# Performance work log

Hardware: AMD Instinct MI355X
Metric: run time of the kernel (lower is better)

The kernel has to match this reference:

```python
import jax, jax.numpy as jnp
import numpy as np

B, T, C = 4, 2048, 1024
E, D, TOP_K = 8, 3072, 2


def setup_inputs() -> dict:
    key = jax.random.key(0)
    ks = jax.random.split(key, 6)
    s_c = 1.0 / np.sqrt(C)
    s_d = 1.0 / np.sqrt(D)
    return {
        "x": jax.random.normal(ks[0], (B, T, C), dtype=jnp.float32),
        "router_w": jax.random.uniform(ks[1], (E, C), jnp.float32, -s_c, s_c),
        "W1": jax.random.uniform(ks[2], (E, C, D), jnp.float32, -s_c, s_c),
        "b1": jax.random.uniform(ks[3], (E, D), jnp.float32, -s_c, s_c),
        "W2": jax.random.uniform(ks[4], (E, D, C), jnp.float32, -s_d, s_d),
        "b2": jax.random.uniform(ks[5], (E, C), jnp.float32, -s_d, s_d),
    }


def reference(x, router_w, W1, b1, W2, b2):
    b, t, c = x.shape
    xf = x.reshape(b * t, c)                      # [N, C]
    n = xf.shape[0]
    logits = xf @ router_w.T                       # [N, E]
    probs = jax.nn.softmax(logits, axis=-1)
    topw, topi = jax.lax.top_k(probs, TOP_K)       # [N, k]
    topw = topw / jnp.sum(topw, axis=-1, keepdims=True)
    # scatter normalized top-k weights into [N, E] combine weights
    mask = jnp.zeros_like(probs).at[jnp.arange(n)[:, None], topi].set(topw)
    # dense expert MLPs (zero combine weight == token not routed to expert)
    h = jax.nn.gelu(jnp.einsum('nc,ecd->ned', xf, W1) + b1, approximate=False)
    y = jnp.einsum('ned,edc->nec', h, W2) + b2     # [N, E, C]
    out = jnp.einsum('ne,nec->nc', mask, y).reshape(b, t, c)
    aux_loss = jnp.zeros((), dtype=x.dtype)        # eval mode
    return out, aux_loss
```

## Files before the change

kernel.cpp:

```cpp
#include <hip/hip_runtime.h>
#include <math.h>

#define N_TOK 8192
#define C_DIM 1024
#define D_DIM 3072
#define E_NUM 8
#define SEG 128
#define MAXB 136

typedef unsigned short u16;
typedef unsigned int u32;
typedef __attribute__((ext_vector_type(8))) short bf16x8;
typedef __attribute__((ext_vector_type(4))) float f32x4;

__device__ __forceinline__ u16 f2bf(float f) {
  u32 u = __builtin_bit_cast(unsigned int, f);
  u = (u + 0x7FFFu + ((u >> 16) & 1u)) >> 16;
  return (u16)u;
}

__global__ void zcnt_kernel(float* __restrict__ out, int n, int* __restrict__ cnt) {
  if (threadIdx.x < E_NUM) cnt[threadIdx.x] = 0;
  const int tail = n & 3;
  if (threadIdx.x < tail) out[n - 1 - (int)threadIdx.x] = 0.0f;
}

__global__ void router_kernel(const float* __restrict__ x, const float* __restrict__ rw,
                              int* __restrict__ cnt, int* __restrict__ list,
                              float* __restrict__ wl, float* __restrict__ out) {
  const int lane = threadIdx.x & 63;
  const int n = blockIdx.x * 4 + (threadIdx.x >> 6);
  {
    float4 z = make_float4(0.f, 0.f, 0.f, 0.f);
    float* orow = out + (size_t)n * C_DIM;
#pragma unroll
    for (int i = 0; i < 4; i++) *(float4*)(orow + lane * 4 + i * 256) = z;
  }
  const float* xr = x + (size_t)n * C_DIM;
  double acc[E_NUM];
#pragma unroll
  for (int e = 0; e < E_NUM; e++) acc[e] = 0.0;
#pragma unroll
  for (int i = 0; i < 4; i++) {
    const int c = lane * 4 + i * 256;
    float4 xv = *(const float4*)(xr + c);
#pragma unroll
    for (int e = 0; e < E_NUM; e++) {
      const float* rwe = rw + e * C_DIM + c;
      acc[e] += (double)xv.x * (double)rwe[0] + (double)xv.y * (double)rwe[1]
              + (double)xv.z * (double)rwe[2] + (double)xv.w * (double)rwe[3];
    }
  }
#pragma unroll
  for (int e = 0; e < E_NUM; e++) {
    double v = acc[e];
#pragma unroll
    for (int off = 32; off > 0; off >>= 1) v += __shfl_down(v, off, 64);
    acc[e] = v;
  }
  if (lane == 0) {
    int i0 = 0;
#pragma unroll
    for (int e = 1; e < E_NUM; e++) if (acc[e] > acc[i0]) i0 = e;
    int i1 = (i0 == 0) ? 1 : 0;
#pragma unroll
    for (int e = 0; e < E_NUM; e++) if (e != i0 && acc[e] > acc[i1]) i1 = e;
    double d = acc[i0] - acc[i1];
    double w0 = 1.0 / (1.0 + exp(-d));
    double w1 = 1.0 - w0;
    int p0 = atomicAdd(&cnt[i0], 1);
    list[i0 * N_TOK + p0] = n; wl[i0 * N_TOK + p0] = (float)w0;
    int p1 = atomicAdd(&cnt[i1], 1);
    list[i1 * N_TOK + p1] = n; wl[i1 * N_TOK + p1] = (float)w1;
  }
}

template<int R, int CC>
__global__ __launch_bounds__(512) void transpose_conv_kernel(
    const float* __restrict__ in, u16* __restrict__ outp) {
  __shared__ float t[32][257];
  const int e = blockIdx.z;
  const int r0 = blockIdx.y * 32;
  const int c0 = blockIdx.x * 256;
  const int tid = threadIdx.x;
  const int lr = tid >> 6;
  const int lc = (tid & 63) * 4;
#pragma unroll
  for (int i = 0; i < 4; i++) {
    const int rr = lr + i * 8;
    float4 v = *(const float4*)(in + ((size_t)e * R + r0 + rr) * CC + c0 + lc);
    t[rr][lc] = v.x; t[rr][lc + 1] = v.y; t[rr][lc + 2] = v.z; t[rr][lc + 3] = v.w;
  }
  __syncthreads();
  const int od = tid >> 1;
  const int seg = (tid & 1) * 16;
  union { u16 s[16]; uint4 v[2]; } o;
#pragma unroll
  for (int j = 0; j < 16; j++) o.s[j] = f2bf(t[seg + j][od]);
  u16* dst = outp + ((size_t)e * CC + c0 + od) * R + r0 + seg;
  *(uint4*)(dst) = o.v[0];
  *(uint4*)(dst + 8) = o.v[1];
}

__global__ void prefix_kernel(const int* __restrict__ cnt, int* __restrict__ rowbase,
                              int* __restrict__ btab) {
  const int lane = threadIdx.x;
  int c[E_NUM], rbse[E_NUM], nseg[E_NUM], nsb[E_NUM];
  int s = 0, t = 0;
#pragma unroll
  for (int e = 0; e < E_NUM; e++) {
    c[e] = cnt[e]; rbse[e] = s; s += c[e];
    nseg[e] = (c[e] + SEG - 1) / SEG; nsb[e] = t; t += nseg[e];
  }
  if (lane < E_NUM) rowbase[lane] = rbse[lane];
  for (int i = lane; i < MAXB; i += 64) {
    int e = -1, m0 = 0;
#pragma unroll
    for (int k = 0; k < E_NUM; k++)
      if (i >= nsb[k] && i < nsb[k] + nseg[k]) { e = k; m0 = (i - nsb[k]) * SEG; }
    btab[2 * i] = e; btab[2 * i + 1] = m0;
  }
}

__global__ void gather_x_kernel(const float* __restrict__ x, const int* __restrict__ rowbase,
                                const int* __restrict__ list, u16* __restrict__ Xg) {
  const int rflat = blockIdx.x * 4 + (threadIdx.x >> 6);
  const int lane = threadIdx.x & 63;
  int e = E_NUM - 1;
#pragma unroll
  for (int k = 1; k < E_NUM; k++) if (rflat < rowbase[k]) { e = k - 1; break; }
  const int p = rflat - rowbase[e];
  const int tok = list[e * N_TOK + p];
  const float* src = x + (size_t)tok * C_DIM;
  u16* dst = Xg + (size_t)rflat * C_DIM;
#pragma unroll
  for (int i = 0; i < 4; i++) {
    float4 v = *(const float4*)(src + lane * 4 + i * 256);
    ushort4 o;
    o.x = f2bf(v.x); o.y = f2bf(v.y); o.z = f2bf(v.z); o.w = f2bf(v.w);
    *(ushort4*)(dst + lane * 4 + i * 256) = o;
  }
}

template<int NN0, int K, int EPI>
__global__ __launch_bounds__(256, 4) void gemm_rs_kernel(
    const u16* __restrict__ A, const u16* __restrict__ Wt, const float* __restrict__ bias_,
    const int* __restrict__ btab, const int* __restrict__ cnt, const int* __restrict__ rowbase,
    const int* __restrict__ list, const float* __restrict__ wl,
    u16* __restrict__ hout, float* __restrict__ out) {
  constexpr int NTOT = NN0 * 128;
  constexpr int NT = K / 32;
  constexpr int NG = NN0 / 4;
  constexpr int TOT = MAXB * NN0;

  __shared__ __align__(16) u16 ldsA[2 * 128 * 32];
  __shared__ __align__(16) u16 ldsB[2 * 128 * 32];

  const int L = (blockIdx.x & 7) * (TOT / 8) + (blockIdx.x >> 3);
  const int coh = L >> 4, r = L & 15;
  const int bxg = coh / NG;
  const int n0g = coh % NG;
  const int bx = bxg * 4 + (r & 3);
  const int n0 = (n0g * 4 + (r >> 2)) * 128;

  const int e = btab[bx * 2];
  if (e < 0) return;
  const int m0 = btab[bx * 2 + 1];
  const int count = cnt[e];
  const int rb = rowbase[e];

  const int tid = threadIdx.x;
  const int lane = tid & 63;
  const int wid = tid >> 6;
  const int wm = (wid >> 1) * 64;
  const int wn = (wid & 1) * 64;
  const int l15 = lane & 15, l4 = lane >> 4;

  const int arow0 = tid >> 2, pos = (tid & 3) * 8;
  const u16* aptr0 = A + (size_t)(rb + min(m0 + arow0, count - 1)) * K + pos;
  const u16* aptr1 = A + (size_t)(rb + min(m0 + arow0 + 64, count - 1)) * K + pos;
  const u16* bptr0 = Wt + ((size_t)e * NTOT + n0 + arow0) * K + pos;
  const u16* bptr1 = Wt + ((size_t)e * NTOT + n0 + arow0 + 64) * K + pos;

  const int paoff = (wm + l15) * 32 + l4 * 8;
  const int pboff = (wn + l15) * 32 + l4 * 8;

  f32x4 acc[4][4];
#pragma unroll
  for (int i = 0; i < 4; i++)
#pragma unroll
    for (int j = 0; j < 4; j++) acc[i][j] = {0.f, 0.f, 0.f, 0.f};

  uint4 ra0, ra1, rb0, rb1;
  auto LOAD = [&](int t) {
    const int ko = t * 32;
    ra0 = *(const uint4*)(aptr0 + ko);
    ra1 = *(const uint4*)(aptr1 + ko);
    rb0 = *(const uint4*)(bptr0 + ko);
    rb1 = *(const uint4*)(bptr1 + ko);
  };
  auto WRITE = [&](int b) {
    *(uint4*)(ldsA + b * 4096 + tid * 8) = ra0;
    *(uint4*)(ldsA + b * 4096 + 2048 + tid * 8) = ra1;
    *(uint4*)(ldsB + b * 4096 + tid * 8) = rb0;
    *(uint4*)(ldsB + b * 4096 + 2048 + tid * 8) = rb1;
  };

  auto PHASE = [&](int b) {
    const u16* pa = ldsA + b * 4096 + paoff;
    const u16* pb = ldsB + b * 4096 + pboff;
    bf16x8 av[4], bv[4];
#pragma unroll
    for (int i = 0; i < 4; i++) av[i] = *(const bf16x8*)(pa + i * 512);
#pragma unroll
    for (int j = 0; j < 4; j++) bv[j] = *(const bf16x8*)(pb + j * 512);
#pragma unroll
    for (int i = 0; i < 4; i++)
#pragma unroll
      for (int j = 0; j < 4; j++)
        acc[i][j] = __builtin_amdgcn_mfma_f32_16x16x32_bf16(av[i], bv[j], acc[i][j], 0, 0, 0);
  };

  LOAD(0);
  WRITE(0);
  asm volatile("s_waitcnt lgkmcnt(0)");
  __builtin_amdgcn_sched_barrier(0);

  for (int t = 0; t < NT - 1; ++t) {
    LOAD(t + 1);
    __builtin_amdgcn_s_barrier();
    __builtin_amdgcn_sched_barrier(0);
    PHASE(t & 1);
    __builtin_amdgcn_s_barrier();
    WRITE((t + 1) & 1);
    asm volatile("s_waitcnt lgkmcnt(0)");
    __builtin_amdgcn_sched_barrier(0);
  }
  __builtin_amdgcn_s_barrier();
  __builtin_amdgcn_sched_barrier(0);
  PHASE((NT - 1) & 1);

  if constexpr (EPI == 1) {
#pragma unroll
    for (int i = 0; i < 4; i++) {
      const int rloc = wm + i * 16 + l4 * 4;
#pragma unroll
      for (int j = 0; j < 4; j++) {
        const int col = n0 + wn + j * 16 + l15;
        const float bias = bias_[e * NTOT + col];
#pragma unroll
        for (int rr = 0; rr < 4; rr++) {
          const int m = m0 + rloc + rr;
          if (m < count) {
            float v = acc[i][j][rr] + bias;
            float g = 0.5f * v * (1.0f + erff(v * 0.70710678118654752f));
            hout[(size_t)(rb + m) * D_DIM + col] = f2bf(g);
          }
        }
      }
    }
  } else {
    const int* lst = list + e * N_TOK;
    const float* wlst = wl + e * N_TOK;
#pragma unroll
    for (int i = 0; i < 4; i++) {
      const int rloc = wm + i * 16 + l4 * 4;
#pragma unroll
      for (int j = 0; j < 4; j++) {
        const int col = n0 + wn + j * 16 + l15;
        const float bias = bias_[e * NTOT + col];
#pragma unroll
        for (int rr = 0; rr < 4; rr++) {
          const int m = m0 + rloc + rr;
          if (m < count) {
            const int tk = lst[m];
            atomicAdd(out + (size_t)tk * C_DIM + col, wlst[m] * (acc[i][j][rr] + bias));
          }
        }
      }
    }
  }
}

extern "C" void kernel_launch(void* const* d_in, const int* in_sizes, int n_in,
                              void* d_out, int out_size, void* d_ws, size_t ws_size,
                              hipStream_t stream) {
  const float* x  = (const float*)d_in[0];
  const float* rw = (const float*)d_in[1];
  const float* W1 = (const float*)d_in[2];
  const float* b1 = (const float*)d_in[3];
  const float* W2 = (const float*)d_in[4];
  const float* b2 = (const float*)d_in[5];
  float* out = (float*)d_out;

  char* ws = (char*)d_ws;
  u16* W1t    = (u16*)(ws);
  u16* Xg     = (u16*)(ws + 50331648);
  u16* W2t    = (u16*)(ws + 50331648);
  int* cnt    = (int*)(ws + 100663296);
  int* rowbase= (int*)(ws + 100663552);
  int* list   = (int*)(ws + 100663808);
  float* wl   = (float*)(ws + 100925952);
  int* btab   = (int*)(ws + 101188096);
  u16* h      = (u16*)(ws + 101190656);

  zcnt_kernel<<<1, 64, 0, stream>>>(out, out_size, cnt);
  router_kernel<<<N_TOK / 4, 256, 0, stream>>>(x, rw, cnt, list, wl, out);
  prefix_kernel<<<1, 64, 0, stream>>>(cnt, rowbase, btab);
  gather_x_kernel<<<(2 * N_TOK) / 4, 256, 0, stream>>>(x, rowbase, list, Xg);
  transpose_conv_kernel<C_DIM, D_DIM><<<dim3(D_DIM / 256, C_DIM / 32, E_NUM), 512, 0, stream>>>(W1, W1t);
  gemm_rs_kernel<24, C_DIM, 1><<<MAXB * 24, 256, 0, stream>>>(
      Xg, W1t, b1, btab, cnt, rowbase, list, wl, h, out);
  transpose_conv_kernel<D_DIM, C_DIM><<<dim3(C_DIM / 256, D_DIM / 32, E_NUM), 512, 0, stream>>>(W2, W2t);
  gemm_rs_kernel<8, D_DIM, 2><<<MAXB * 8, 256, 0, stream>>>(
      h, W2t, b2, btab, cnt, rowbase, list, wl, h, out);
}
```

Baseline: 653.7 us.

## Use direct global-to-LDS loads with triple-buffered pipeline in expert GEMMs

Replaces the register-staged global loads plus LDS writes with global_load_lds direct-to-LDS transfers. The double buffer becomes a triple buffer so two K-tiles are in flight while the current one is computed, synchronised with vmcnt waits. This is meant to cut VGPR pressure and LDS write instructions and to hide more memory latency. In exchange LDS use per block rises by half, which may reduce occupancy, and correctness depends on the vmcnt accounting.

```diff
diff --git a/kernel.cpp b/kernel.cpp
--- a/kernel.cpp
+++ b/kernel.cpp
@@ -17,6 +17,12 @@
   u32 u = __builtin_bit_cast(unsigned int, f);
   u = (u + 0x7FFFu + ((u >> 16) & 1u)) >> 16;
   return (u16)u;
+}
+
+__device__ __forceinline__ void gl_lds16(const void* g, void* l) {
+  __builtin_amdgcn_global_load_lds(
+      (const __attribute__((address_space(1))) unsigned int*)g,
+      (__attribute__((address_space(3))) unsigned int*)l, 16, 0, 0);
 }
 
 __global__ void zcnt_kernel(float* __restrict__ out, int n, int* __restrict__ cnt) {
@@ -143,7 +149,7 @@
 }
 
 template<int NN0, int K, int EPI>
-__global__ __launch_bounds__(256, 4) void gemm_rs_kernel(
+__global__ __launch_bounds__(256, 4) void gemm_d3_kernel(
     const u16* __restrict__ A, const u16* __restrict__ Wt, const float* __restrict__ bias_,
     const int* __restrict__ btab, const int* __restrict__ cnt, const int* __restrict__ rowbase,
     const int* __restrict__ list, const float* __restrict__ wl,
@@ -153,8 +159,8 @@
   constexpr int NG = NN0 / 4;
   constexpr int TOT = MAXB * NN0;
 
-  __shared__ __align__(16) u16 ldsA[2 * 128 * 32];
-  __shared__ __align__(16) u16 ldsB[2 * 128 * 32];
+  __shared__ __align__(16) u16 ldsA[3 * 128 * 32];
+  __shared__ __align__(16) u16 ldsB[3 * 128 * 32];
 
   const int L = (blockIdx.x & 7) * (TOT / 8) + (blockIdx.x >> 3);
   const int coh = L >> 4, r = L & 15;
@@ -191,24 +197,19 @@
 #pragma unroll
     for (int j = 0; j < 4; j++) acc[i][j] = {0.f, 0.f, 0.f, 0.f};
 
-  uint4 ra0, ra1, rb0, rb1;
-  auto LOAD = [&](int t) {
+  auto STAGE = [&](int t) {
+    const int s = (t % 3) * 4096;
     const int ko = t * 32;
-    ra0 = *(const uint4*)(aptr0 + ko);
-    ra1 = *(const uint4*)(aptr1 + ko);
-    rb0 = *(const uint4*)(bptr0 + ko);
-    rb1 = *(const uint4*)(bptr1 + ko);
+    gl_lds16(aptr0 + ko, ldsA + s + tid * 8);
+    gl_lds16(aptr1 + ko, ldsA + s + 2048 + tid * 8);
+    gl_lds16(bptr0 + ko, ldsB + s + tid * 8);
+    gl_lds16(bptr1 + ko, ldsB + s + 2048 + tid * 8);
   };
-  auto WRITE = [&](int b) {
-    *(uint4*)(ldsA + b * 4096 + tid * 8) = ra0;
-    *(uint4*)(ldsA + b * 4096 + 2048 + tid * 8) = ra1;
-    *(uint4*)(ldsB + b * 4096 + tid * 8) = rb0;
-    *(uint4*)(ldsB + b * 4096 + 2048 + tid * 8) = rb1;
-  };
-
-  auto PHASE = [&](int b) {
-    const u16* pa = ldsA + b * 4096 + paoff;
-    const u16* pb = ldsB + b * 4096 + pboff;
+
+  auto PHASE = [&](int t) {
+    const int s = (t % 3) * 4096;
+    const u16* pa = ldsA + s + paoff;
+    const u16* pb = ldsB + s + pboff;
     bf16x8 av[4], bv[4];
 #pragma unroll
     for (int i = 0; i < 4; i++) av[i] = *(const bf16x8*)(pa + i * 512);
@@ -221,24 +222,29 @@
         acc[i][j] = __builtin_amdgcn_mfma_f32_16x16x32_bf16(av[i], bv[j], acc[i][j], 0, 0, 0);
   };
 
-  LOAD(0);
-  WRITE(0);
-  asm volatile("s_waitcnt lgkmcnt(0)");
-  __builtin_amdgcn_sched_barrier(0);
-
-  for (int t = 0; t < NT - 1; ++t) {
-    LOAD(t + 1);
+  STAGE(0); STAGE(1);
+  for (int t = 0; t < NT - 2; ++t) {
+    STAGE(t + 2);
+    asm volatile("s_waitcnt vmcnt(8)");
+    __builtin_amdgcn_sched_barrier(0);
     __builtin_amdgcn_s_barrier();
     __builtin_amdgcn_sched_barrier(0);
-    PHASE(t & 1);
+    PHASE(t);
     __builtin_amdgcn_s_barrier();
-    WRITE((t + 1) & 1);
-    asm volatile("s_waitcnt lgkmcnt(0)");
     __builtin_amdgcn_sched_barrier(0);
   }
+  asm volatile("s_waitcnt vmcnt(4)");
+  __builtin_amdgcn_sched_barrier(0);
   __builtin_amdgcn_s_barrier();
   __builtin_amdgcn_sched_barrier(0);
-  PHASE((NT - 1) & 1);
+  PHASE(NT - 2);
+  __builtin_amdgcn_s_barrier();
+  __builtin_amdgcn_sched_barrier(0);
+  asm volatile("s_waitcnt vmcnt(0)");
+  __builtin_amdgcn_sched_barrier(0);
+  __builtin_amdgcn_s_barrier();
+  __builtin_amdgcn_sched_barrier(0);
+  PHASE(NT - 1);
 
   if constexpr (EPI == 1) {
 #pragma unroll
@@ -309,9 +315,9 @@
   prefix_kernel<<<1, 64, 0, stream>>>(cnt, rowbase, btab);
   gather_x_kernel<<<(2 * N_TOK) / 4, 256, 0, stream>>>(x, rowbase, list, Xg);
   transpose_conv_kernel<C_DIM, D_DIM><<<dim3(D_DIM / 256, C_DIM / 32, E_NUM), 512, 0, stream>>>(W1, W1t);
-  gemm_rs_kernel<24, C_DIM, 1><<<MAXB * 24, 256, 0, stream>>>(
+  gemm_d3_kernel<24, C_DIM, 1><<<MAXB * 24, 256, 0, stream>>>(
       Xg, W1t, b1, btab, cnt, rowbase, list, wl, h, out);
   transpose_conv_kernel<D_DIM, C_DIM><<<dim3(C_DIM / 256, D_DIM / 32, E_NUM), 512, 0, stream>>>(W2, W2t);
-  gemm_rs_kernel<8, D_DIM, 2><<<MAXB * 8, 256, 0, stream>>>(
+  gemm_d3_kernel<8, D_DIM, 2><<<MAXB * 8, 256, 0, stream>>>(
       h, W2t, b2, btab, cnt, rowbase, list, wl, h, out);
 }
```

Result: slower. 689.4 us (+5.5%).
